# Optimization experiments

Hardware: AMD Instinct MI355X
Metric: run time of the kernel (lower is better)

Reference implementation:

```python
import jax, jax.numpy as jnp
import numpy as np
from jax import lax

B, S, V, E, H = 128, 256, 50000, 300, 512
Hh = H // 2  # per-direction hidden


def _lstm_dir(x, Wih, Whh, bih, bhh):
    # x: [B,S,E] -> hs: [B,S,Hh]; PyTorch gate order i,f,g,o
    b = x.shape[0]
    h0 = jnp.zeros((b, Hh), x.dtype)
    c0 = jnp.zeros((b, Hh), x.dtype)
    bias = bih + bhh

    def step(carry, xt):
        h, c = carry
        g = xt @ Wih.T + h @ Whh.T + bias  # [B,4Hh]
        i, f, gg, o = jnp.split(g, 4, axis=-1)
        c = jax.nn.sigmoid(f) * c + jax.nn.sigmoid(i) * jnp.tanh(gg)
        h = jax.nn.sigmoid(o) * jnp.tanh(c)
        return (h, c), h

    _, hs = lax.scan(step, (h0, c0), jnp.swapaxes(x, 0, 1))
    return jnp.swapaxes(hs, 0, 1)


def _bilstm(x, p):
    fwd = _lstm_dir(x, p['Wih_f'], p['Whh_f'], p['bih_f'], p['bhh_f'])
    bwd = _lstm_dir(jnp.flip(x, 1), p['Wih_b'], p['Whh_b'], p['bih_b'], p['bhh_b'])
    return jnp.concatenate([fwd, jnp.flip(bwd, 1)], axis=-1)  # [B,S,H]


def _masked_mean(h, length_minus1):
    # mean over first (len-1) timesteps, vectorized replacement for per-sample loop
    mask = (jnp.arange(h.shape[1])[None, :] < length_minus1[:, None]).astype(h.dtype)  # [B,S]
    return jnp.einsum('bsh,bs->bh', h, mask) / length_minus1[:, None].astype(h.dtype)


def setup_inputs() -> dict:
    key = jax.random.key(0)
    ks = jax.random.split(key, 20)
    sc = 0.05
    inp = {
        'x1': jax.random.randint(ks[0], (B, S), 0, V, dtype=jnp.int32),
        'x2': jax.random.randint(ks[1], (B, S), 0, V, dtype=jnp.int32),
        'len1': jax.random.randint(ks[2], (B,), 2, S + 1, dtype=jnp.int32),
        'len2': jax.random.randint(ks[3], (B,), 2, S + 1, dtype=jnp.int32),
        'emb': jax.random.normal(ks[4], (V, E), jnp.float32) * sc,
        'Wih_f': jax.random.normal(ks[5], (4 * Hh, E), jnp.float32) * sc,
        'Whh_f': jax.random.normal(ks[6], (4 * Hh, Hh), jnp.float32) * sc,
        'bih_f': jnp.zeros((4 * Hh,), jnp.float32),
        'bhh_f': jnp.zeros((4 * Hh,), jnp.float32),
        'Wih_b': jax.random.normal(ks[7], (4 * Hh, E), jnp.float32) * sc,
        'Whh_b': jax.random.normal(ks[8], (4 * Hh, Hh), jnp.float32) * sc,
        'bih_b': jnp.zeros((4 * Hh,), jnp.float32),
        'bhh_b': jnp.zeros((4 * Hh,), jnp.float32),
        'W1': jax.random.normal(ks[9], (H, H), jnp.float32) * sc,
        'b1': jnp.zeros((H,), jnp.float32),
        'W2': jax.random.normal(ks[10], (H // 2, H), jnp.float32) * sc,
        'b2': jnp.zeros((H // 2,), jnp.float32),
        'Wo': jax.random.normal(ks[11], (1, H // 2), jnp.float32) * sc,
        'bo': jnp.zeros((1,), jnp.float32),
    }
    return inp


def reference(x1, x2, len1, len2, emb, Wih_f, Whh_f, bih_f, bhh_f,
              Wih_b, Whh_b, bih_b, bhh_b, W1, b1, W2, b2, Wo, bo):
    p = dict(Wih_f=Wih_f, Whh_f=Whh_f, bih_f=bih_f, bhh_f=bhh_f,
             Wih_b=Wih_b, Whh_b=Whh_b, bih_b=bih_b, bhh_b=bhh_b)
    e1 = emb[x1]  # [B,S,E]
    e2 = emb[x2]
    h1 = _bilstm(e1, p)  # [B,S,H]
    h2 = _bilstm(e2, p)
    v1 = _masked_mean(h1, len1 - 1)  # [B,H]
    v2 = _masked_mean(h2, len2 - 1)
    vec = jnp.abs(v1 - v2)  # aggr_type == 'sub'
    a1 = jax.nn.relu(vec @ W1.T + b1)
    a2 = jax.nn.relu(a1 @ W2.T + b2)
    logits = (a2 @ Wo.T + bo)[:, 0]  # [B]
    preds = jax.nn.sigmoid(logits)
    return logits, preds
```

## Files before the change

### kernel.cpp

```cpp
#include <hip/hip_runtime.h>
#include <hip/hip_bf16.h>
#include <math.h>

typedef unsigned short u16;
typedef short s16x8 __attribute__((ext_vector_type(8)));
typedef float f32x4v __attribute__((ext_vector_type(4)));
typedef int i32x4 __attribute__((ext_vector_type(4)));
typedef unsigned short u16x4 __attribute__((ext_vector_type(4)));

#define EDIM 300
#define EPAD 320
#define VOCAB 50000

static constexpr size_t SZ_WIH  = (size_t)2 * 1024 * EPAD * 2;
static constexpr size_t SZ_WPK  = (size_t)2 * 1024 * 256;
static constexpr size_t SZ_SW   = (size_t)2 * 1024 * 4;
static constexpr size_t SZ_BIAS = (size_t)2 * 1024 * 4;
static constexpr size_t SZ_HSV  = (size_t)2 * 256 * 256;
static constexpr size_t SZ_CST  = (size_t)2 * 256 * 256 * 4;
static constexpr size_t SZ_VAC  = (size_t)2 * 256 * 256 * 4;
static constexpr size_t SZ_VOUT = (size_t)2 * 128 * 512 * 4;
static constexpr size_t SZ_EMB  = (size_t)VOCAB * EPAD * 2;
static constexpr size_t SZ_PAD  = (size_t)512 * 1024;
static constexpr size_t FIXED_B = SZ_WIH + SZ_WPK + SZ_SW + SZ_BIAS + SZ_HSV + SZ_CST + SZ_VAC + SZ_VOUT + SZ_EMB + SZ_PAD;
static constexpr size_t PER_T   = (size_t)512 * 1024 * 2;


__device__ __forceinline__ float bf2f(u16 u) {
  union { float f; unsigned int i; } v; v.i = ((unsigned int)u) << 16; return v.f;
}
__device__ __forceinline__ u16 f2bf(float f) {
  union { float f; unsigned int i; } v; v.f = f;
  unsigned int r = v.i + 0x7fffu + ((v.i >> 16) & 1u);
  return (u16)(r >> 16);
}
__device__ __forceinline__ void gload_lds16(const void* g, void* l) {
  __builtin_amdgcn_global_load_lds((const __attribute__((address_space(1))) void*)g,
                                   (__attribute__((address_space(3))) void*)l, 16, 0, 0);
}
__device__ __forceinline__ void lds_barrier() {
  asm volatile("s_waitcnt lgkmcnt(0)" ::: "memory");
  __builtin_amdgcn_s_barrier();
}
__device__ __forceinline__ void wave_lds_fence() {
  asm volatile("s_waitcnt lgkmcnt(0)" ::: "memory");
  __builtin_amdgcn_sched_barrier(0);
}

__global__ void prep_kernel(const float* wih_f, const float* bih_f, const float* bhh_f,
                            const float* wih_b, const float* bih_b, const float* bhh_b,
                            u16* wih_bf, float* bias)
{
  int tid = blockIdx.x * blockDim.x + threadIdx.x;
  if (tid < 2 * 1024 * EPAD) {
    int d = tid / (1024 * EPAD); int rr = tid % (1024 * EPAD);
    int p = rr / EPAD; int k = rr % EPAD;
    int w = p >> 7, q = (p >> 4) & 7, ul = p & 15;
    int jlog = (q & 3) * 256 + w * 32 + (q >> 2) * 16 + ul;
    const float* wsrc = d ? wih_b : wih_f;
    wih_bf[tid] = (k < EDIM) ? f2bf(wsrc[(size_t)jlog * EDIM + k]) : (u16)0;
  }
  int t2 = tid - 2 * 1024 * EPAD;
  if (t2 >= 0 && t2 < 2 * 1024) {
    int d = t2 >> 10; int p = t2 & 1023;
    int w = p >> 7, q = (p >> 4) & 7, ul = p & 15;
    int jlog = (q & 3) * 256 + w * 32 + (q >> 2) * 16 + ul;
    bias[t2] = d ? (bih_b[jlog] + bhh_b[jlog]) : (bih_f[jlog] + bhh_f[jlog]);
  }
}

__global__ void embconv_kernel(const float* emb, u16* embbf)
{
  int r = blockIdx.x;
  int k = threadIdx.x;
  embbf[(size_t)r * EPAD + k] = (k < EDIM) ? f2bf(emb[(size_t)r * EDIM + k]) : (u16)0;
}

__global__ void whhq_kernel(const float* whh_f, const float* whh_b, char* wpk, float* sw)
{
  int jp = blockIdx.x;
  int t = threadIdx.x;
  int d = jp >> 10, p = jp & 1023;
  int w = p >> 7, q = (p >> 4) & 7, ul = p & 15;
  int jlog = (q & 3) * 256 + w * 32 + (q >> 2) * 16 + ul;
  const float* src = (d ? whh_b : whh_f) + (size_t)jlog * 256;
  float v[4]; float m = 0.f;
  #pragma unroll
  for (int kk = 0; kk < 4; ++kk) { v[kk] = src[t * 4 + kk]; m = fmaxf(m, fabsf(v[kk])); }
  #pragma unroll
  for (int off = 32; off > 0; off >>= 1) m = fmaxf(m, __shfl_xor(m, off));
  float sunit = m / 127.f;
  if (sunit < 1e-30f) sunit = 1e-30f;
  unsigned int pk = 0;
  #pragma unroll
  for (int kk = 0; kk < 4; ++kk) {
    int qv = (int)rintf(v[kk] / sunit);
    qv = qv > 127 ? 127 : (qv < -127 ? -127 : qv);
    pk |= ((unsigned int)(qv & 255)) << (8 * kk);
  }
  size_t base = ((((size_t)(d * 8 + w) * 8 + q) * 4 + (t >> 4)) * 64
                 + (((t >> 2) & 3) * 16 + ul)) * 16 + (t & 3) * 4;
  *(unsigned int*)&wpk[base] = pk;
  if (t == 0) sw[jp] = sunit / 127.f;
}

__global__ void __launch_bounds__(512, 1)
gemm_chunk_kernel(const int* __restrict__ x1, const int* __restrict__ x2,
                  const u16* __restrict__ embbf, const u16* __restrict__ wih_bf,
                  const float* __restrict__ bias, u16* __restrict__ ginc,
                  int t0, int T, int logT)
{
  __shared__ __align__(16) u16 As[5 * 8192];
  __shared__ __align__(16) u16 Bs[2 * 8192];

  int m0 = blockIdx.x * 128;
  int d  = m0 >> (8 + logT);
  int tl = (m0 >> 8) & (T - 1);
  int R0 = m0 & 255;
  int lane = threadIdx.x & 63;
  int w = threadIdx.x >> 6;
  int wm = w >> 1, wn = w & 1;

  const int* x = (R0 >> 7) ? x2 : x1;
  int t = t0 + tl;
  int tpos = d ? (255 - t) : t;

  int ar  = lane >> 3;
  int acb = (lane & 7) * 16;
  int swz = ar << 4;

  int toks[2];
  #pragma unroll
  for (int i = 0; i < 2; ++i) {
    int lrow = (i * 8 + w) * 8 + ar;
    toks[i] = x[((R0 + lrow) & 127) * 256 + tpos];
  }

  const char* Bbase = (const char*)(wih_bf + (size_t)d * 1024 * EPAD);
  const char* Ebase = (const char*)embbf;

  #pragma unroll
  for (int kt = 0; kt < 5; ++kt)
    #pragma unroll
    for (int i = 0; i < 2; ++i)
      gload_lds16(Ebase + (size_t)toks[i] * 640 + kt * 128 + (acb ^ swz),
                  (char*)As + kt * 16384 + (i * 8 + w) * 1024);
  #pragma unroll
  for (int i = 0; i < 2; ++i) {
    int lrow = (i * 8 + w) * 8 + ar;
    gload_lds16(Bbase + (size_t)lrow * 640 + (acb ^ swz),
                (char*)Bs + (i * 8 + w) * 1024);
  }
  __syncthreads();

  size_t rowbase = (size_t)(d * T + tl) * 256 + R0;
  int buf = 0;

  for (int nt = 0; nt < 8; ++nt) {
    f32x4v acc[2][4] = {};
    for (int kt = 0; kt < 5; ++kt) {
      int nkt = kt + 1, nnt = nt;
      if (nkt == 5) { nkt = 0; nnt = nt + 1; }
      if (nnt < 8) {
        #pragma unroll
        for (int i = 0; i < 2; ++i) {
          int lrow = nnt * 128 + (i * 8 + w) * 8 + ar;
          gload_lds16(Bbase + (size_t)lrow * 640 + nkt * 128 + (acb ^ swz),
                      (char*)Bs + (buf ^ 1) * 16384 + (i * 8 + w) * 1024);
        }
      }
      #pragma unroll
      for (int kc = 0; kc < 2; ++kc) {
        s16x8 a[2], b[4];
        int cb = kc * 64 + (lane >> 4) * 16;
        #pragma unroll
        for (int mf = 0; mf < 2; ++mf) {
          int rr = wm * 32 + mf * 16 + (lane & 15);
          a[mf] = *(const s16x8*)((const char*)As + kt * 16384 + rr * 128 + (cb ^ ((rr & 7) << 4)));
        }
        #pragma unroll
        for (int nf = 0; nf < 4; ++nf) {
          int rr = wn * 64 + nf * 16 + (lane & 15);
          b[nf] = *(const s16x8*)((const char*)Bs + buf * 16384 + rr * 128 + (cb ^ ((rr & 7) << 4)));
        }
        #pragma unroll
        for (int mf = 0; mf < 2; ++mf)
          #pragma unroll
          for (int nf = 0; nf < 4; ++nf)
            acc[mf][nf] = __builtin_amdgcn_mfma_f32_16x16x32_bf16(a[mf], b[nf], acc[mf][nf], 0, 0, 0);
      }
      __syncthreads();
      buf ^= 1;
    }

    float bv[4];
    #pragma unroll
    for (int nf = 0; nf < 4; ++nf)
      bv[nf] = bias[d * 1024 + nt * 128 + wn * 64 + nf * 16 + (lane & 15)];
    int scol = nt * 128 + wn * 64 + (lane & 15) * 4;
    #pragma unroll
    for (int mf = 0; mf < 2; ++mf)
      #pragma unroll
      for (int i = 0; i < 4; ++i) {
        int row = wm * 32 + mf * 16 + (lane >> 4) * 4 + i;
        u16x4 v;
        #pragma unroll
        for (int nf = 0; nf < 4; ++nf)
          v[nf] = f2bf(acc[mf][nf][i] + bv[nf]);
        *(u16x4*)(ginc + (rowbase + row) * 1024 + scol) = v;
      }
  }
}

__global__ void __launch_bounds__(512)
lstm_chunk_kernel(const u16* __restrict__ ginc, const i32x4* __restrict__ wpk,
                  const float* __restrict__ sw, char* hsave,
                  float* cstate, float* vaccst, float* vout,
                  const int* len1, const int* len2, int t0, int T)
{
  __shared__ __align__(16) char h_lds[2][2][288];
  __shared__ __align__(16) int gstage[8][64][4];

  const int bid = blockIdx.x;
  const int d = bid >> 7, bt = bid & 127;
  const int tid = threadIdx.x;
  const int lane = tid & 63, w = tid >> 6;
  const int cl = lane & 15;

  const int cr  = lane >> 5;
  const int cuh = (lane >> 4) & 1;
  const int cu  = w * 32 + cuh * 16 + cl;

  i32x4 bfr[8][4];
  #pragma unroll
  for (int q = 0; q < 8; ++q)
    #pragma unroll
    for (int kc = 0; kc < 4; ++kc)
      bfr[q][kc] = wpk[(((size_t)(d * 8 + w) * 8 + q) * 4 + kc) * 64 + lane];
  float swl4[4];
  #pragma unroll
  for (int g = 0; g < 4; ++g)
    swl4[g] = sw[d * 1024 + w * 128 + (cuh * 4 + g) * 16 + cl];

  const int R0 = bt * 2;
  {
    int r = tid >> 8, u = tid & 255;
    h_lds[0][r][u] = (t0 > 0) ? hsave[((size_t)d * 256 + R0 + r) * 256 + u] : (char)0;
  }

  const int RR = R0 + cr;
  const int lm = ((RR >> 7) ? len2 : len1)[RR & 127] - 1;
  const size_t sidx = ((size_t)d * 256 + RR) * 256 + cu;
  float c = 0.f, va = 0.f;
  if (t0 > 0) { c = cstate[sidx]; va = vaccst[sidx]; }

  const size_t GSTEP = (size_t)256 * 1024;
  const u16* gcell = ginc + ((size_t)d * T * 256 + RR) * 1024 + w * 128 + cuh * 64 + cl * 4;
  u16x4 gv = *(const u16x4*)gcell;
  __syncthreads();

  const bool final_chunk = (t0 + T == 256);
  int par = 0;

  for (int tl = 0; tl < T; ++tl) {
    u16x4 gvn = *(const u16x4*)(gcell + GSTEP * (size_t)(tl + 1));

    i32x4 a[4] = {{0,0,0,0},{0,0,0,0},{0,0,0,0},{0,0,0,0}};
    if (cl < 2) {
      #pragma unroll
      for (int kc = 0; kc < 4; ++kc)
        a[kc] = *(const i32x4*)&h_lds[par][cl][kc * 64 + (lane >> 4) * 16];
    }
    i32x4 acc[8];
    #pragma unroll
    for (int q = 0; q < 8; ++q) {
      i32x4 z = {0, 0, 0, 0};
      #pragma unroll
      for (int kc = 0; kc < 4; ++kc)
        z = __builtin_amdgcn_mfma_i32_16x16x64_i8(a[kc], bfr[q][kc], z, 0, 0, 0);
      acc[q] = z;
    }

    if (lane < 16) {
      #pragma unroll
      for (int r2 = 0; r2 < 2; ++r2)
        #pragma unroll
        for (int uh2 = 0; uh2 < 2; ++uh2) {
          i32x4 v = { acc[uh2 * 4 + 0][r2], acc[uh2 * 4 + 1][r2],
                      acc[uh2 * 4 + 2][r2], acc[uh2 * 4 + 3][r2] };
          *(i32x4*)&gstage[w][r2 * 32 + uh2 * 16 + lane][0] = v;
        }
    }
    wave_lds_fence();
    i32x4 g4 = *(const i32x4*)&gstage[w][lane][0];

    {
      float s0 = (float)g4[0] * swl4[0] + bf2f(gv[0]);
      float s1 = (float)g4[1] * swl4[1] + bf2f(gv[1]);
      float s2 = (float)g4[2] * swl4[2] + bf2f(gv[2]);
      float s3 = (float)g4[3] * swl4[3] + bf2f(gv[3]);
      float I = __builtin_amdgcn_rcpf(1.f + __expf(-s0));
      float F = __builtin_amdgcn_rcpf(1.f + __expf(-s1));
      float G = 1.f - 2.f * __builtin_amdgcn_rcpf(__expf(2.f * s2) + 1.f);
      float O = __builtin_amdgcn_rcpf(1.f + __expf(-s3));
      float cn = F * c + I * G;
      c = cn;
      float hn = O * (1.f - 2.f * __builtin_amdgcn_rcpf(__expf(2.f * cn) + 1.f));
      int tmap = d ? (255 - (t0 + tl)) : (t0 + tl);
      if (tmap < lm) va += hn;
      h_lds[par ^ 1][cr][cu] = (char)(int)rintf(hn * 127.f);
    }
    lds_barrier();
    gv = gvn;
    par ^= 1;
  }

  cstate[sidx] = c;
  vaccst[sidx] = va;
  if (final_chunk) {
    vout[((size_t)(RR >> 7) * 128 + (RR & 127)) * 512 + d * 256 + cu] = va / (float)lm;
  } else {
    int r = tid >> 8, u = tid & 255;
    hsave[((size_t)d * 256 + R0 + r) * 256 + u] = h_lds[par][r][u];
  }
}

__global__ void mlp_kernel(const float* v, const float* W1, const float* b1,
                           const float* W2, const float* b2, const float* Wo, const float* bo,
                           float* out)
{
  __shared__ float vec[512];
  __shared__ float a1[512];
  __shared__ float red[4];
  int b = blockIdx.x;
  int tid = threadIdx.x;
  for (int i = tid; i < 512; i += 256)
    vec[i] = fabsf(v[(size_t)b * 512 + i] - v[(size_t)(128 + b) * 512 + i]);
  __syncthreads();
  for (int j = tid; j < 512; j += 256) {
    float s = b1[j];
    const float* wr = W1 + (size_t)j * 512;
    for (int k = 0; k < 512; ++k) s += vec[k] * wr[k];
    a1[j] = fmaxf(s, 0.f);
  }
  __syncthreads();
  float s = b2[tid];
  {
    const float* wr = W2 + (size_t)tid * 512;
    for (int k = 0; k < 512; ++k) s += a1[k] * wr[k];
  }
  float p = fmaxf(s, 0.f) * Wo[tid];
  for (int off = 32; off > 0; off >>= 1) p += __shfl_down(p, off);
  if ((tid & 63) == 0) red[tid >> 6] = p;
  __syncthreads();
  if (tid == 0) {
    float logit = red[0] + red[1] + red[2] + red[3] + bo[0];
    out[b] = logit;
    out[128 + b] = 1.f / (1.f + __expf(-logit));
  }
}

extern "C" void kernel_launch(void* const* d_in, const int* in_sizes, int n_in,
                              void* d_out, int out_size, void* d_ws, size_t ws_size,
                              hipStream_t stream)
{
  const int*   x1    = (const int*)d_in[0];
  const int*   x2    = (const int*)d_in[1];
  const int*   len1  = (const int*)d_in[2];
  const int*   len2  = (const int*)d_in[3];
  const float* emb   = (const float*)d_in[4];
  const float* wih_f = (const float*)d_in[5];
  const float* whh_f = (const float*)d_in[6];
  const float* bih_f = (const float*)d_in[7];
  const float* bhh_f = (const float*)d_in[8];
  const float* wih_b = (const float*)d_in[9];
  const float* whh_b = (const float*)d_in[10];
  const float* bih_b = (const float*)d_in[11];
  const float* bhh_b = (const float*)d_in[12];
  const float* W1    = (const float*)d_in[13];
  const float* b1    = (const float*)d_in[14];
  const float* W2    = (const float*)d_in[15];
  const float* b2    = (const float*)d_in[16];
  const float* Wo    = (const float*)d_in[17];
  const float* bo    = (const float*)d_in[18];

  char* p = (char*)d_ws;
  u16*   wih_bf = (u16*)p;          p += SZ_WIH;
  char*  wpk    = (char*)p;         p += SZ_WPK;
  float* swp    = (float*)p;        p += SZ_SW;
  float* bias   = (float*)p;        p += SZ_BIAS;
  char*  hsave  = (char*)p;         p += SZ_HSV;
  float* cst    = (float*)p;        p += SZ_CST;
  float* vac    = (float*)p;        p += SZ_VAC;
  float* vout   = (float*)p;        p += SZ_VOUT;
  u16*   embbf  = (u16*)p;          p += SZ_EMB;

  int T = 256;
  while (T > 1 && FIXED_B + (size_t)T * PER_T > ws_size) T >>= 1;
  int logT = __builtin_ctz((unsigned)T);
  u16* ginc = (u16*)p;

  {
    int total = 2 * 1024 * EPAD + 2 * 1024;
    prep_kernel<<<(total + 255) / 256, 256, 0, stream>>>(
        wih_f, bih_f, bhh_f, wih_b, bih_b, bhh_b, wih_bf, bias);
  }
  whhq_kernel<<<2048, 64, 0, stream>>>(whh_f, whh_b, wpk, swp);
  embconv_kernel<<<VOCAB, EPAD, 0, stream>>>(emb, embbf);

  int nch = 256 / T;
  for (int ch = 0; ch < nch; ++ch) {
    int tt0 = ch * T;
    gemm_chunk_kernel<<<dim3(4 * T), 512, 0, stream>>>(x1, x2, embbf, wih_bf, bias,
                                                       ginc, tt0, T, logT);
    lstm_chunk_kernel<<<256, 512, 0, stream>>>(ginc, (const i32x4*)wpk, swp, hsave,
                                               cst, vac, vout, len1, len2, tt0, T);
  }

  mlp_kernel<<<128, 256, 0, stream>>>(vout, W1, b1, W2, b2, Wo, bo, (float*)d_out);
}
```

Measured before the change: 480.6 us.

## Fuse input GEMM and LSTM recurrence into one kernel with double-buffered chunk slabs

Merges the per-chunk input-projection GEMM and the LSTM recurrence into a single launch. In each launch, the LSTM blocks process chunk i-1 while the GEMM blocks compute chunk i into the other of two alternating slabs, so the latency-bound recurrence overlaps with the throughput-bound GEMM. The GEMM body is also reworked: each wave holds its 16 embedding rows in registers instead of staging A tiles in LDS, which cuts shared memory use so more blocks fit per CU. The two slabs double the gate workspace, which may force a smaller chunk size. Co-resident GEMM blocks can also contend with the recurrence for CU resources.

```diff
diff --git a/kernel.cpp b/kernel.cpp
--- a/kernel.cpp
+++ b/kernel.cpp
@@ -23,7 +23,7 @@
 static constexpr size_t SZ_EMB  = (size_t)VOCAB * EPAD * 2;
 static constexpr size_t SZ_PAD  = (size_t)512 * 1024;
 static constexpr size_t FIXED_B = SZ_WIH + SZ_WPK + SZ_SW + SZ_BIAS + SZ_HSV + SZ_CST + SZ_VAC + SZ_VOUT + SZ_EMB + SZ_PAD;
-static constexpr size_t PER_T   = (size_t)512 * 1024 * 2;
+static constexpr size_t SZ_STEP = (size_t)2 * 256 * 1024 * 2;
 
 
 __device__ __forceinline__ float bf2f(u16 u) {
@@ -104,47 +104,36 @@
   if (t == 0) sw[jp] = sunit / 127.f;
 }
 
-__global__ void __launch_bounds__(512, 1)
-gemm_chunk_kernel(const int* __restrict__ x1, const int* __restrict__ x2,
-                  const u16* __restrict__ embbf, const u16* __restrict__ wih_bf,
-                  const float* __restrict__ bias, u16* __restrict__ ginc,
-                  int t0, int T, int logT)
-{
-  __shared__ __align__(16) u16 As[5 * 8192];
-  __shared__ __align__(16) u16 Bs[2 * 8192];
-
-  int m0 = blockIdx.x * 128;
-  int d  = m0 >> (8 + logT);
-  int tl = (m0 >> 8) & (T - 1);
-  int R0 = m0 & 255;
+__device__ __forceinline__ void gemm_body(
+    int bid, const int* __restrict__ x1, const int* __restrict__ x2,
+    const u16* __restrict__ embbf, const u16* __restrict__ wih_bf,
+    const float* __restrict__ bias, u16* __restrict__ slab,
+    int t0, int T, int logT, char* smem)
+{
+  u16* Bs = (u16*)smem;
+  int d  = bid >> (1 + logT);
+  int tl = (bid >> 1) & (T - 1);
+  int R0 = (bid & 1) * 128;
   int lane = threadIdx.x & 63;
   int w = threadIdx.x >> 6;
-  int wm = w >> 1, wn = w & 1;
 
   const int* x = (R0 >> 7) ? x2 : x1;
   int t = t0 + tl;
   int tpos = d ? (255 - t) : t;
 
+  int rowR = R0 + w * 16 + (lane & 15);
+  int tok = x[(rowR & 127) * 256 + tpos];
+  const char* arow = (const char*)embbf + (size_t)tok * 640 + (lane >> 4) * 16;
+  s16x8 areg[10];
+  #pragma unroll
+  for (int kc = 0; kc < 10; ++kc)
+    areg[kc] = *(const s16x8*)(arow + kc * 64);
+
+  const char* Bbase = (const char*)(wih_bf + (size_t)d * 1024 * EPAD);
   int ar  = lane >> 3;
   int acb = (lane & 7) * 16;
   int swz = ar << 4;
 
-  int toks[2];
-  #pragma unroll
-  for (int i = 0; i < 2; ++i) {
-    int lrow = (i * 8 + w) * 8 + ar;
-    toks[i] = x[((R0 + lrow) & 127) * 256 + tpos];
-  }
-
-  const char* Bbase = (const char*)(wih_bf + (size_t)d * 1024 * EPAD);
-  const char* Ebase = (const char*)embbf;
-
-  #pragma unroll
-  for (int kt = 0; kt < 5; ++kt)
-    #pragma unroll
-    for (int i = 0; i < 2; ++i)
-      gload_lds16(Ebase + (size_t)toks[i] * 640 + kt * 128 + (acb ^ swz),
-                  (char*)As + kt * 16384 + (i * 8 + w) * 1024);
   #pragma unroll
   for (int i = 0; i < 2; ++i) {
     int lrow = (i * 8 + w) * 8 + ar;
@@ -155,78 +144,67 @@
 
   size_t rowbase = (size_t)(d * T + tl) * 256 + R0;
   int buf = 0;
+  int ul = lane & 15;
 
   for (int nt = 0; nt < 8; ++nt) {
-    f32x4v acc[2][4] = {};
+    f32x4v acc[8] = {};
+    #pragma unroll
     for (int kt = 0; kt < 5; ++kt) {
       int nkt = kt + 1, nnt = nt;
       if (nkt == 5) { nkt = 0; nnt = nt + 1; }
       if (nnt < 8) {
         #pragma unroll
         for (int i = 0; i < 2; ++i) {
-          int lrow = nnt * 128 + (i * 8 + w) * 8 + ar;
-          gload_lds16(Bbase + (size_t)lrow * 640 + nkt * 128 + (acb ^ swz),
+          int lrow = (i * 8 + w) * 8 + ar;
+          gload_lds16(Bbase + (size_t)(nnt * 128 + lrow) * 640 + nkt * 128 + (acb ^ swz),
                       (char*)Bs + (buf ^ 1) * 16384 + (i * 8 + w) * 1024);
         }
       }
       #pragma unroll
-      for (int kc = 0; kc < 2; ++kc) {
-        s16x8 a[2], b[4];
-        int cb = kc * 64 + (lane >> 4) * 16;
+      for (int kc2 = 0; kc2 < 2; ++kc2) {
+        int cb = kc2 * 64 + (lane >> 4) * 16;
         #pragma unroll
-        for (int mf = 0; mf < 2; ++mf) {
-          int rr = wm * 32 + mf * 16 + (lane & 15);
-          a[mf] = *(const s16x8*)((const char*)As + kt * 16384 + rr * 128 + (cb ^ ((rr & 7) << 4)));
+        for (int nf = 0; nf < 8; ++nf) {
+          int rr = nf * 16 + (lane & 15);
+          s16x8 b = *(const s16x8*)((const char*)Bs + buf * 16384 + rr * 128 + (cb ^ ((rr & 7) << 4)));
+          acc[nf] = __builtin_amdgcn_mfma_f32_16x16x32_bf16(areg[kt * 2 + kc2], b, acc[nf], 0, 0, 0);
         }
-        #pragma unroll
-        for (int nf = 0; nf < 4; ++nf) {
-          int rr = wn * 64 + nf * 16 + (lane & 15);
-          b[nf] = *(const s16x8*)((const char*)Bs + buf * 16384 + rr * 128 + (cb ^ ((rr & 7) << 4)));
-        }
-        #pragma unroll
-        for (int mf = 0; mf < 2; ++mf)
-          #pragma unroll
-          for (int nf = 0; nf < 4; ++nf)
-            acc[mf][nf] = __builtin_amdgcn_mfma_f32_16x16x32_bf16(a[mf], b[nf], acc[mf][nf], 0, 0, 0);
       }
       __syncthreads();
       buf ^= 1;
     }
-
-    float bv[4];
+    float bv[8];
     #pragma unroll
-    for (int nf = 0; nf < 4; ++nf)
-      bv[nf] = bias[d * 1024 + nt * 128 + wn * 64 + nf * 16 + (lane & 15)];
-    int scol = nt * 128 + wn * 64 + (lane & 15) * 4;
+    for (int nf = 0; nf < 8; ++nf)
+      bv[nf] = bias[d * 1024 + nt * 128 + nf * 16 + ul];
     #pragma unroll
-    for (int mf = 0; mf < 2; ++mf)
+    for (int uh = 0; uh < 2; ++uh)
       #pragma unroll
       for (int i = 0; i < 4; ++i) {
-        int row = wm * 32 + mf * 16 + (lane >> 4) * 4 + i;
+        int row = w * 16 + (lane >> 4) * 4 + i;
         u16x4 v;
         #pragma unroll
-        for (int nf = 0; nf < 4; ++nf)
-          v[nf] = f2bf(acc[mf][nf][i] + bv[nf]);
-        *(u16x4*)(ginc + (rowbase + row) * 1024 + scol) = v;
+        for (int g = 0; g < 4; ++g)
+          v[g] = f2bf(acc[uh * 4 + g][i] + bv[uh * 4 + g]);
+        *(u16x4*)(slab + (rowbase + row) * 1024 + nt * 128 + uh * 64 + ul * 4) = v;
       }
   }
 }
 
-__global__ void __launch_bounds__(512)
-lstm_chunk_kernel(const u16* __restrict__ ginc, const i32x4* __restrict__ wpk,
-                  const float* __restrict__ sw, char* hsave,
-                  float* cstate, float* vaccst, float* vout,
-                  const int* len1, const int* len2, int t0, int T)
-{
-  __shared__ __align__(16) char h_lds[2][2][288];
-  __shared__ __align__(16) int gstage[8][64][4];
-
-  const int bid = blockIdx.x;
+__device__ __forceinline__ void lstm_body(
+    int bid, const u16* __restrict__ slab, const i32x4* __restrict__ wpk,
+    const float* __restrict__ sw, char* hsave,
+    float* cstate, float* vaccst, float* vout,
+    const int* __restrict__ len1, const int* __restrict__ len2,
+    int t0, int T, char* smem)
+{
+  char* h = smem;
+  int* gst = (int*)(smem + 1152);
+
   const int d = bid >> 7, bt = bid & 127;
   const int tid = threadIdx.x;
   const int lane = tid & 63, w = tid >> 6;
   const int cl = lane & 15;
-
   const int cr  = lane >> 5;
   const int cuh = (lane >> 4) & 1;
   const int cu  = w * 32 + cuh * 16 + cl;
@@ -245,7 +223,7 @@
   const int R0 = bt * 2;
   {
     int r = tid >> 8, u = tid & 255;
-    h_lds[0][r][u] = (t0 > 0) ? hsave[((size_t)d * 256 + R0 + r) * 256 + u] : (char)0;
+    h[r * 288 + u] = (t0 > 0) ? hsave[((size_t)d * 256 + R0 + r) * 256 + u] : (char)0;
   }
 
   const int RR = R0 + cr;
@@ -255,7 +233,7 @@
   if (t0 > 0) { c = cstate[sidx]; va = vaccst[sidx]; }
 
   const size_t GSTEP = (size_t)256 * 1024;
-  const u16* gcell = ginc + ((size_t)d * T * 256 + RR) * 1024 + w * 128 + cuh * 64 + cl * 4;
+  const u16* gcell = slab + ((size_t)d * T * 256 + RR) * 1024 + w * 128 + cuh * 64 + cl * 4;
   u16x4 gv = *(const u16x4*)gcell;
   __syncthreads();
 
@@ -269,7 +247,7 @@
     if (cl < 2) {
       #pragma unroll
       for (int kc = 0; kc < 4; ++kc)
-        a[kc] = *(const i32x4*)&h_lds[par][cl][kc * 64 + (lane >> 4) * 16];
+        a[kc] = *(const i32x4*)&h[(par * 2 + cl) * 288 + kc * 64 + (lane >> 4) * 16];
     }
     i32x4 acc[8];
     #pragma unroll
@@ -288,11 +266,11 @@
         for (int uh2 = 0; uh2 < 2; ++uh2) {
           i32x4 v = { acc[uh2 * 4 + 0][r2], acc[uh2 * 4 + 1][r2],
                       acc[uh2 * 4 + 2][r2], acc[uh2 * 4 + 3][r2] };
-          *(i32x4*)&gstage[w][r2 * 32 + uh2 * 16 + lane][0] = v;
+          *(i32x4*)&gst[(w * 64 + r2 * 32 + uh2 * 16 + lane) * 4] = v;
         }
     }
     wave_lds_fence();
-    i32x4 g4 = *(const i32x4*)&gstage[w][lane][0];
+    i32x4 g4 = *(const i32x4*)&gst[(w * 64 + lane) * 4];
 
     {
       float s0 = (float)g4[0] * swl4[0] + bf2f(gv[0]);
@@ -308,7 +286,7 @@
       float hn = O * (1.f - 2.f * __builtin_amdgcn_rcpf(__expf(2.f * cn) + 1.f));
       int tmap = d ? (255 - (t0 + tl)) : (t0 + tl);
       if (tmap < lm) va += hn;
-      h_lds[par ^ 1][cr][cu] = (char)(int)rintf(hn * 127.f);
+      h[((par ^ 1) * 2 + cr) * 288 + cu] = (char)(int)rintf(hn * 127.f);
     }
     lds_barrier();
     gv = gvn;
@@ -321,7 +299,25 @@
     vout[((size_t)(RR >> 7) * 128 + (RR & 127)) * 512 + d * 256 + cu] = va / (float)lm;
   } else {
     int r = tid >> 8, u = tid & 255;
-    hsave[((size_t)d * 256 + R0 + r) * 256 + u] = h_lds[par][r][u];
+    hsave[((size_t)d * 256 + R0 + r) * 256 + u] = h[(par * 2 + r) * 288 + u];
+  }
+}
+
+__global__ void __launch_bounds__(512, 4)
+fused_kernel(const int* x1, const int* x2, const u16* embbf, const u16* wih_bf,
+             const float* bias, const i32x4* wpk, const float* sw,
+             char* hsave, float* cstate, float* vaccst, float* vout,
+             const int* len1, const int* len2,
+             const u16* lstm_slab, u16* gemm_slab,
+             int lstm_t0, int gemm_t0, int nL, int T, int logT)
+{
+  __shared__ __align__(16) char smem[32768];
+  if ((int)blockIdx.x < nL) {
+    lstm_body(blockIdx.x, lstm_slab, wpk, sw, hsave, cstate, vaccst, vout,
+              len1, len2, lstm_t0, T, smem);
+  } else if (gemm_t0 >= 0) {
+    gemm_body(blockIdx.x - nL, x1, x2, embbf, wih_bf, bias, gemm_slab,
+              gemm_t0, T, logT, smem);
   }
 }
 
@@ -396,9 +392,11 @@
   u16*   embbf  = (u16*)p;          p += SZ_EMB;
 
   int T = 256;
-  while (T > 1 && FIXED_B + (size_t)T * PER_T > ws_size) T >>= 1;
+  while (T > 1 && FIXED_B + (size_t)2 * T * SZ_STEP > ws_size) T >>= 1;
   int logT = __builtin_ctz((unsigned)T);
-  u16* ginc = (u16*)p;
+  u16* slab0 = (u16*)p;             p += (size_t)T * SZ_STEP;
+  u16* slab1 = (u16*)p;
+  u16* slabs[2] = { slab0, slab1 };
 
   {
     int total = 2 * 1024 * EPAD + 2 * 1024;
@@ -408,14 +406,21 @@
   whhq_kernel<<<2048, 64, 0, stream>>>(whh_f, whh_b, wpk, swp);
   embconv_kernel<<<VOCAB, EPAD, 0, stream>>>(emb, embbf);
 
-  int nch = 256 / T;
-  for (int ch = 0; ch < nch; ++ch) {
-    int tt0 = ch * T;
-    gemm_chunk_kernel<<<dim3(4 * T), 512, 0, stream>>>(x1, x2, embbf, wih_bf, bias,
-                                                       ginc, tt0, T, logT);
-    lstm_chunk_kernel<<<256, 512, 0, stream>>>(ginc, (const i32x4*)wpk, swp, hsave,
-                                               cst, vac, vout, len1, len2, tt0, T);
-  }
+  int NCH = 256 / T;
+  fused_kernel<<<4 * T, 512, 0, stream>>>(x1, x2, embbf, wih_bf, bias,
+                                          (const i32x4*)wpk, swp, hsave, cst, vac, vout,
+                                          len1, len2, slabs[0], slabs[0],
+                                          -1, 0, 0, T, logT);
+  for (int ch = 1; ch < NCH; ++ch) {
+    fused_kernel<<<256 + 4 * T, 512, 0, stream>>>(x1, x2, embbf, wih_bf, bias,
+                                                  (const i32x4*)wpk, swp, hsave, cst, vac, vout,
+                                                  len1, len2, slabs[(ch - 1) & 1], slabs[ch & 1],
+                                                  (ch - 1) * T, ch * T, 256, T, logT);
+  }
+  fused_kernel<<<256, 512, 0, stream>>>(x1, x2, embbf, wih_bf, bias,
+                                        (const i32x4*)wpk, swp, hsave, cst, vac, vout,
+                                        len1, len2, slabs[(NCH - 1) & 1], slabs[0],
+                                        (NCH - 1) * T, -1, 256, T, logT);
 
   mlp_kernel<<<128, 256, 0, stream>>>(vout, W1, b1, W2, b2, Wo, bo, (float*)d_out);
 }
```

Measured after the change: 1.266 ms. +163.5%, slower.
